# Kernel tuning notes

Measured on AMD Instinct MI355X. Metric: run time of the kernel, lower is better.

## Reference

```python
import jax, jax.numpy as jnp
import numpy as np
from jax import lax

B_, N_, DIM, HEADS, WS, HW = 16, 3136, 512, 8, 7, 56
SD = DIM // 2          # single_dim per branch (mul=[1,1])
S = SD // HEADS        # per-branch head dim


def setup_inputs() -> dict:
    key = jax.random.key(0)
    ks = jax.random.split(key, 12)
    r = lambda i, shape, sc=0.02: jax.random.normal(ks[i], shape, jnp.float32) * sc
    return dict(
        x=jax.random.normal(ks[0], (B_, N_, DIM), jnp.float32),
        H=HW, W=HW,
        q_w=r(1, (DIM, DIM)),
        kv_dw_w=r(2, (DIM, 1, 3, 3), 0.3), kv_dw_b=jnp.zeros((DIM,), jnp.float32),
        kv_pw_w=r(3, (DIM, DIM, 1, 1), 0.05), kv_pw_b=jnp.zeros((DIM,), jnp.float32),
        fc_w0=r(4, (S, S)), fc_w1=r(5, (S, S)),
        single_w0=r(6, (2 * S, S)), single_w1=r(7, (2 * S, S)),
        local_w0=r(8, (SD, 1, 3, 3), 0.3), local_b0=jnp.zeros((SD,), jnp.float32),
        local_w1=r(9, (SD, 1, 3, 3), 0.3), local_b1=jnp.zeros((SD,), jnp.float32),
        proj_w=r(10, (DIM, DIM)), proj_b=jnp.zeros((DIM,), jnp.float32),
    )


def _dwconv(x, w, b):
    # depthwise 3x3, padding 1 (NCHW / OIHW)
    y = lax.conv_general_dilated(x, w, (1, 1), [(1, 1), (1, 1)],
                                 feature_group_count=x.shape[1],
                                 dimension_numbers=('NCHW', 'OIHW', 'NCHW'))
    return y + b[None, :, None, None]


def _pwconv(x, w, b):
    y = lax.conv_general_dilated(x, w, (1, 1), [(0, 0), (0, 0)],
                                 dimension_numbers=('NCHW', 'OIHW', 'NCHW'))
    return y + b[None, :, None, None]


def _unfold(x, k, stride, dil):
    # nn.Unfold(kernel_size=k, stride=stride, padding=0, dilation=dil): [B,C,H,W] -> [B, C*k*k, L]
    B, C, H, W = x.shape
    L = (H - (dil * (k - 1) + 1)) // stride + 1  # H == W here
    idx = (jnp.arange(L) * stride)[:, None] + jnp.arange(k) * dil  # [L, k]
    t = x[:, :, idx, :]            # [B,C,Lh,kh,W]
    t = t[:, :, :, :, idx]         # [B,C,Lh,kh,Lw,kw]
    t = t.transpose(0, 1, 3, 5, 2, 4)  # [B,C,kh,kw,Lh,Lw] -> torch unfold channel order
    return t.reshape(B, C * k * k, L * L)


def reference(x, H, W, q_w, kv_dw_w, kv_dw_b, kv_pw_w, kv_pw_b,
              fc_w0, fc_w1, single_w0, single_w1,
              local_w0, local_b0, local_w1, local_b1, proj_w, proj_b):
    B, N, C = x.shape
    q = (x @ q_w.T).reshape(B, N, HEADS, C // HEADS).transpose(0, 2, 1, 3)  # [B,h,N,C/h]
    xim = x.reshape(B, H, W, C).transpose(0, 3, 1, 2)
    kv = _pwconv(_dwconv(xim, kv_dw_w, kv_dw_b), kv_pw_w, kv_pw_b)  # [B,C,H,W]
    branches = [(fc_w0, single_w0, local_w0, local_b0),
                (fc_w1, single_w1, local_w1, local_b1)]
    outs = []
    for i, (fc_w, single_w, lw, lb) in enumerate(branches):
        dil = 2 ** i
        stride = dil * (WS - 1) + 1
        q_ = q[:, :, :, i * S:(i + 1) * S]                      # [B,h,N,S]
        u = _unfold(kv[:, i * SD:(i + 1) * SD], WS, stride, dil)  # [B, SD*49, L]
        L = u.shape[-1]
        u = u.reshape(B, HEADS, S, WS * WS, L).transpose(0, 1, 3, 4, 2)  # [B,h,49,L,S]
        u = u.reshape(B, HEADS, WS * WS, L * S)
        # AdaptiveAvgPool2d((None, S)): mean over consecutive chunks of length L
        pooled = u.reshape(B, HEADS, WS * WS, S, L).mean(-1)     # [B,h,49,S]
        kvp = (pooled @ fc_w.T) @ single_w.T                     # [B,h,49,2S]
        k_, v_ = kvp[..., :S], kvp[..., S:]
        attn = jax.nn.softmax((q_ @ k_.transpose(0, 1, 3, 2)) * (S ** -0.5), axis=-1)  # [B,h,N,49]
        vimg = v_.transpose(0, 1, 3, 2).reshape(B, SD, WS, WS)
        v_ = v_ + _dwconv(vimg, lw, lb).reshape(B, HEADS, S, WS * WS).transpose(0, 1, 3, 2)
        outs.append((attn @ v_).transpose(0, 2, 1, 3).reshape(B, N, SD))
    return jnp.concatenate(outs, -1) @ proj_w.T + proj_b
```

## Files before the change

kernel.cpp:

```cpp
#include <hip/hip_runtime.h>


typedef _Float16 __attribute__((ext_vector_type(8))) f16x8;
typedef _Float16 __attribute__((ext_vector_type(4))) f16x4;
typedef float __attribute__((ext_vector_type(4))) f32x4;

#define NB    16
#define NTOK  3136
#define CDIM  512
#define HWDIM 56
#define SLICE 100352

__device__ __forceinline__ void gll16(const void* g, void* l) {
    __builtin_amdgcn_global_load_lds((const __attribute__((address_space(1))) void*)g,
                                     (__attribute__((address_space(3))) void*)l, 16, 0, 0);
}

__global__ __launch_bounds__(256) void cast_f2h(const float* __restrict__ in,
                                                _Float16* __restrict__ out, int n8) {
    int i = blockIdx.x * 256 + threadIdx.x;
    if (i >= n8) return;
    const float4* p = (const float4*)in + (size_t)i * 2;
    float4 a = p[0], b = p[1];
    f16x8 o;
    o[0] = (_Float16)a.x; o[1] = (_Float16)a.y; o[2] = (_Float16)a.z; o[3] = (_Float16)a.w;
    o[4] = (_Float16)b.x; o[5] = (_Float16)b.y; o[6] = (_Float16)b.z; o[7] = (_Float16)b.w;
    *(f16x8*)(out + (size_t)i * 8) = o;
}

__global__ __launch_bounds__(256) void prep(const float* __restrict__ q_w,
                                            const float* __restrict__ pw_w,
                                            const float* __restrict__ pj_w,
                                            const float* __restrict__ dw_w,
                                            _Float16* __restrict__ WQ,
                                            _Float16* __restrict__ WPW,
                                            _Float16* __restrict__ WPJ,
                                            float* __restrict__ WT) {
    int bid = blockIdx.x;
    if (bid < 384) {
        const float* src = bid < 128 ? q_w : (bid < 256 ? pw_w : pj_w);
        _Float16* dst = bid < 128 ? WQ : (bid < 256 ? WPW : WPJ);
        int i = (bid & 127) * 256 + threadIdx.x;
        const float4* p = (const float4*)src + (size_t)i * 2;
        float4 a = p[0], b = p[1];
        f16x8 o;
        o[0] = (_Float16)a.x; o[1] = (_Float16)a.y; o[2] = (_Float16)a.z; o[3] = (_Float16)a.w;
        o[4] = (_Float16)b.x; o[5] = (_Float16)b.y; o[6] = (_Float16)b.z; o[7] = (_Float16)b.w;
        *(f16x8*)(dst + (size_t)i * 8) = o;
    } else {
        int i = (bid - 384) * 256 + threadIdx.x;
        if (i < 512 * 9) {
            int c = i / 9, t = i - c * 9;
            WT[t * 512 + c] = dw_w[i];
        }
    }
}

__global__ __launch_bounds__(256) void dwconv3x3(const _Float16* __restrict__ xh,
                                                 const float* __restrict__ wt,
                                                 const float* __restrict__ bias,
                                                 _Float16* __restrict__ out) {
    const int pr = blockIdx.x * 4 + (threadIdx.x >> 6);
    const int c0 = (threadIdx.x & 63) * 8;
    const int b  = pr / (28 * HWDIM);
    const int rm = pr - b * (28 * HWDIM);
    const int hp = rm / HWDIM;
    const int w  = rm - hp * HWDIM;
    const int h0 = hp * 2;

    float wr[9][8];
#pragma unroll
    for (int t = 0; t < 9; ++t) {
        float4 a = *(const float4*)(wt + t * 512 + c0);
        float4 d = *(const float4*)(wt + t * 512 + c0 + 4);
        wr[t][0] = a.x; wr[t][1] = a.y; wr[t][2] = a.z; wr[t][3] = a.w;
        wr[t][4] = d.x; wr[t][5] = d.y; wr[t][6] = d.z; wr[t][7] = d.w;
    }
    float acc0[8], acc1[8];
    {
        float4 a = *(const float4*)(bias + c0);
        float4 d = *(const float4*)(bias + c0 + 4);
        acc0[0] = a.x; acc0[1] = a.y; acc0[2] = a.z; acc0[3] = a.w;
        acc0[4] = d.x; acc0[5] = d.y; acc0[6] = d.z; acc0[7] = d.w;
#pragma unroll
        for (int j = 0; j < 8; ++j) acc1[j] = acc0[j];
    }
#pragma unroll
    for (int rr = 0; rr < 4; ++rr) {
        const int row = h0 - 1 + rr;
        if ((unsigned)row >= HWDIM) continue;
#pragma unroll
        for (int kw = 0; kw < 3; ++kw) {
            const int ww = w + kw - 1;
            if ((unsigned)ww >= HWDIM) continue;
            f16x8 v = *(const f16x8*)(xh + ((size_t)(b * NTOK + row * HWDIM + ww) * CDIM + c0));
            if (rr < 3) {
                const int t = rr * 3 + kw;
#pragma unroll
                for (int j = 0; j < 8; ++j) acc0[j] += (float)v[j] * wr[t][j];
            }
            if (rr > 0) {
                const int t = (rr - 1) * 3 + kw;
#pragma unroll
                for (int j = 0; j < 8; ++j) acc1[j] += (float)v[j] * wr[t][j];
            }
        }
    }
    f16x8 o0, o1;
#pragma unroll
    for (int j = 0; j < 8; ++j) { o0[j] = (_Float16)acc0[j]; o1[j] = (_Float16)acc1[j]; }
    const size_t p0 = (size_t)(b * NTOK + h0 * HWDIM + w) * CDIM + c0;
    *(f16x8*)(out + p0) = o0;
    *(f16x8*)(out + p0 + (size_t)HWDIM * CDIM) = o1;
}

template <int MODE>
__global__ __launch_bounds__(256) void gemm_bt(const _Float16* __restrict__ A,
                                               const _Float16* __restrict__ B,
                                               const float* __restrict__ bias,
                                               _Float16* __restrict__ Ch,
                                               float* __restrict__ Cf,
                                               int M, int N, int K) {
    __shared__ _Float16 As[128 * 64];
    __shared__ _Float16 Bs[128 * 64];
    const int tid = threadIdx.x;
    const int lane = tid & 63;
    const int wave = tid >> 6;
    const size_t m0 = (size_t)blockIdx.x * 128;
    const int n0 = blockIdx.y * 128;
    const int wm = wave >> 1, wn = wave & 1;
    const int lr = lane & 15, lk = lane >> 4;
    const int srow = wave * 8 + (lane >> 3);
    const int scol = (lane & 7) * 8;

    unsigned bj[4], nj[4];
    const int shalf = scol >> 5;
    const int wcol = scol & 31;
    if constexpr (MODE == 2) {
#pragma unroll
        for (int j = 0; j < 4; ++j) {
            unsigned row = (unsigned)m0 + j * 32 + srow;
            bj[j] = row / 3136u;
            nj[j] = row - bj[j] * 3136u;
        }
    }

    f32x4 acc[4][4] = {};
    for (int kt = 0; kt < K; kt += 64) {
        if constexpr (MODE == 2) {
            const int s = (kt >> 5) + shalf;
            const size_t soff = (size_t)s * SLICE + wcol;
#pragma unroll
            for (int j = 0; j < 4; ++j) {
                gll16(A + (size_t)bj[j] * 16 * SLICE + soff + (size_t)nj[j] * 32,
                      &As[j * 2048 + wave * 512]);
                gll16(B + ((size_t)(n0 + j * 32 + srow) * K + kt + scol),
                      &Bs[j * 2048 + wave * 512]);
            }
        } else {
#pragma unroll
            for (int j = 0; j < 4; ++j) {
                gll16(A + ((m0 + j * 32 + srow) * K + kt + scol), &As[j * 2048 + wave * 512]);
                gll16(B + ((size_t)(n0 + j * 32 + srow) * K + kt + scol), &Bs[j * 2048 + wave * 512]);
            }
        }
        __syncthreads();
#pragma unroll
        for (int ks = 0; ks < 2; ++ks) {
            f16x8 af[4], bf[4];
#pragma unroll
            for (int mi = 0; mi < 4; ++mi)
                af[mi] = *(const f16x8*)&As[(wm * 64 + mi * 16 + lr) * 64 + ks * 32 + lk * 8];
#pragma unroll
            for (int ni = 0; ni < 4; ++ni)
                bf[ni] = *(const f16x8*)&Bs[(wn * 64 + ni * 16 + lr) * 64 + ks * 32 + lk * 8];
#pragma unroll
            for (int mi = 0; mi < 4; ++mi)
#pragma unroll
                for (int ni = 0; ni < 4; ++ni)
                    acc[mi][ni] = __builtin_amdgcn_mfma_f32_16x16x32_f16(af[mi], bf[ni], acc[mi][ni], 0, 0, 0);
        }
        __syncthreads();
    }

    if constexpr (MODE == 0) {
#pragma unroll
        for (int mi = 0; mi < 4; ++mi)
#pragma unroll
            for (int ni = 0; ni < 4; ++ni) {
                const int col = n0 + wn * 64 + ni * 16 + lr;
                const int sl = col >> 5, sc = col & 31;
#pragma unroll
                for (int j = 0; j < 4; ++j) {
                    unsigned row = (unsigned)m0 + wm * 64 + mi * 16 + lk * 4 + j;
                    unsigned bb = row / 3136u, nn = row - bb * 3136u;
                    Ch[((size_t)bb * 16 + sl) * SLICE + (size_t)nn * 32 + sc] =
                        (_Float16)acc[mi][ni][j];
                }
            }
    } else {
#pragma unroll
        for (int mi = 0; mi < 4; ++mi)
#pragma unroll
            for (int ni = 0; ni < 4; ++ni) {
                const int col = n0 + wn * 64 + ni * 16 + lr;
                const float bv = bias[col];
#pragma unroll
                for (int j = 0; j < 4; ++j) {
                    const size_t row = m0 + wm * 64 + mi * 16 + lk * 4 + j;
                    float v = acc[mi][ni][j] + bv;
                    if constexpr (MODE == 2) Cf[row * N + col] = v;
                    else Ch[row * N + col] = (_Float16)v;
                }
            }
    }
}

__global__ __launch_bounds__(256) void kv_small(const _Float16* __restrict__ kvh,
                                                const float* __restrict__ fc0, const float* __restrict__ fc1,
                                                const float* __restrict__ sg0, const float* __restrict__ sg1,
                                                const float* __restrict__ lw0, const float* __restrict__ lb0,
                                                const float* __restrict__ lw1, const float* __restrict__ lb1,
                                                _Float16* __restrict__ Kb, _Float16* __restrict__ Vb) {
    const int head = blockIdx.x;
    const int br = blockIdx.y;
    const int b = blockIdx.z;
    const float* fc = br ? fc1 : fc0;
    const float* sg = br ? sg1 : sg0;
    const float* lw = br ? lw1 : lw0;
    const float* lb = br ? lb1 : lb0;
    __shared__ float pooled[49 * 32];
    __shared__ float tmp[49 * 32];
    __shared__ float kvp[49 * 64];
    const int tid = threadIdx.x;
    if (br == 0) {
        for (int idx = tid; idx < 49 * 64; idx += 256) {
            int w = idx >> 6, l = idx & 63;
            int ly = l >> 3, lx = l & 7, pp = w / 7, qq = w % 7;
            int n = (ly * 7 + pp) * HWDIM + (lx * 7 + qq);
            const f16x8* src = (const f16x8*)(kvh + ((size_t)(b * NTOK + n) * CDIM + head * 32));
            float s = 0;
#pragma unroll
            for (int t = 0; t < 4; ++t) {
                f16x8 v = src[t];
#pragma unroll
                for (int j = 0; j < 8; ++j) s += (float)v[j];
            }
            kvp[idx] = s;
        }
        __syncthreads();
        for (int idx = tid; idx < 49 * 32; idx += 256) {
            int w = idx >> 5, sp = idx & 31;
            pooled[idx] = (kvp[(w << 6) + 2 * sp] + kvp[(w << 6) + 2 * sp + 1]) * (1.f / 64.f);
        }
    } else {
        for (int idx = tid; idx < 49 * 32; idx += 256) {
            int w = idx >> 5, t = idx & 31;
            int l = t >> 1, hf = t & 1;
            int ly = l >> 2, lx = l & 3, pp = w / 7, qq = w % 7;
            int n = (ly * 13 + pp * 2) * HWDIM + (lx * 13 + qq * 2);
            const f16x8* src = (const f16x8*)(kvh + ((size_t)(b * NTOK + n) * CDIM + 256 + head * 32 + hf * 16));
            float s = 0;
#pragma unroll
            for (int t2 = 0; t2 < 2; ++t2) {
                f16x8 v = src[t2];
#pragma unroll
                for (int j = 0; j < 8; ++j) s += (float)v[j];
            }
            pooled[idx] = s * (1.f / 16.f);
        }
    }
    __syncthreads();
    for (int idx = tid; idx < 49 * 32; idx += 256) {
        int w = idx >> 5, j = idx & 31;
        float s = 0;
#pragma unroll
        for (int k = 0; k < 32; ++k) s += pooled[(w << 5) + k] * fc[j * 32 + k];
        tmp[idx] = s;
    }
    __syncthreads();
    for (int idx = tid; idx < 49 * 64; idx += 256) {
        int w = idx >> 6, o = idx & 63;
        float s = 0;
#pragma unroll
        for (int k = 0; k < 32; ++k) s += tmp[(w << 5) + k] * sg[o * 32 + k];
        kvp[idx] = s;
    }
    __syncthreads();
    const size_t base = (((size_t)b * 2 + br) * 8 + head) * 1568;
    for (int idx = tid; idx < 49 * 32; idx += 256) {
        int w = idx >> 5, sp = idx & 31;
        Kb[base + idx] = (_Float16)kvp[(w << 6) + sp];
        int pp = w / 7, qq = w % 7;
        int c = head * 32 + sp;
        float a = kvp[(w << 6) + 32 + sp] + lb[c];
#pragma unroll
        for (int kh = 0; kh < 3; ++kh) {
            int p2 = pp + kh - 1;
            if ((unsigned)p2 >= 7) continue;
#pragma unroll
            for (int kw = 0; kw < 3; ++kw) {
                int q2 = qq + kw - 1;
                if ((unsigned)q2 >= 7) continue;
                a += kvp[((p2 * 7 + q2) << 6) + 32 + sp] * lw[c * 9 + kh * 3 + kw];
            }
        }
        Vb[base + idx] = (_Float16)a;
    }
}

__global__ __launch_bounds__(256) void attn_fused(const _Float16* __restrict__ Qp,
                                                  const _Float16* __restrict__ Kb,
                                                  const _Float16* __restrict__ Vb,
                                                  _Float16* __restrict__ AOp) {
    const int b = blockIdx.y;
    const int br = blockIdx.z >> 3;
    const int head = blockIdx.z & 7;
    __shared__ _Float16 Kp[64 * 40];
    __shared__ _Float16 Vt[32 * 72];
    __shared__ _Float16 Pw[4][32 * 72];
    const int tid = threadIdx.x;
    const int lane = tid & 63, wave = tid >> 6;
    const size_t kvbase = (((size_t)b * 2 + br) * 8 + head) * 1568;
    {
        int r = tid >> 2, ck = tid & 3;
        f16x8 v = {};
        if (r < 49) v = *(const f16x8*)(Kb + kvbase + r * 32 + ck * 8);
        *(f16x8*)&Kp[r * 40 + ck * 8] = v;
    }
    for (int idx = tid; idx < 64 * 32; idx += 256) {
        int w = idx >> 5, s = idx & 31;
        Vt[s * 72 + w] = (w < 49) ? Vb[kvbase + w * 32 + s] : (_Float16)0.f;
    }
    __syncthreads();
    const int mtile = blockIdx.x * 4 + wave;
    if (mtile >= 49) return;
    const int n0 = mtile * 64;
    const int lr = lane & 15, lk = lane >> 4;
    const size_t qsl = ((size_t)b * 16 + head * 2 + br) * SLICE + (size_t)n0 * 32;
    const size_t osl = ((size_t)b * 16 + br * 8 + head) * SLICE + (size_t)n0 * 32;

    f16x8 qf[4], kf[4];
#pragma unroll
    for (int mi = 0; mi < 4; ++mi)
        qf[mi] = *(const f16x8*)(Qp + qsl + (size_t)(mi * 16 + lr) * 32 + lk * 8);
#pragma unroll
    for (int ni = 0; ni < 4; ++ni)
        kf[ni] = *(const f16x8*)&Kp[(ni * 16 + lr) * 40 + lk * 8];
    f32x4 sacc[4][4] = {};
#pragma unroll
    for (int mi = 0; mi < 4; ++mi)
#pragma unroll
        for (int ni = 0; ni < 4; ++ni)
            sacc[mi][ni] = __builtin_amdgcn_mfma_f32_16x16x32_f16(qf[mi], kf[ni], sacc[mi][ni], 0, 0, 0);

    float den[4][4];
#pragma unroll
    for (int mi = 0; mi < 4; ++mi)
#pragma unroll
        for (int j = 0; j < 4; ++j) den[mi][j] = 0.f;
    const float SCALE = 0.17677669529663687f;
#pragma unroll
    for (int mi = 0; mi < 4; ++mi)
#pragma unroll
        for (int ni = 0; ni < 4; ++ni) {
            const bool valid = (ni * 16 + lr) < 49;
#pragma unroll
            for (int j = 0; j < 4; ++j) {
                float e = valid ? __expf(sacc[mi][ni][j] * SCALE) : 0.f;
                sacc[mi][ni][j] = e;
                den[mi][j] += e;
            }
        }
#pragma unroll
    for (int mi = 0; mi < 4; ++mi)
#pragma unroll
        for (int j = 0; j < 4; ++j) {
            float d = den[mi][j];
            d += __shfl_xor(d, 1);
            d += __shfl_xor(d, 2);
            d += __shfl_xor(d, 4);
            d += __shfl_xor(d, 8);
            den[mi][j] = 1.f / d;
        }
    f16x4 ph[4][4];
#pragma unroll
    for (int mi = 0; mi < 4; ++mi)
#pragma unroll
        for (int ni = 0; ni < 4; ++ni)
#pragma unroll
            for (int j = 0; j < 4; ++j)
                ph[mi][ni][j] = (_Float16)(sacc[mi][ni][j] * den[mi][j]);

    _Float16* P = Pw[wave];
#pragma unroll
    for (int h = 0; h < 2; ++h) {
#pragma unroll
        for (int mh = 0; mh < 2; ++mh) {
            const int mi = h * 2 + mh;
#pragma unroll
            for (int ni = 0; ni < 4; ++ni)
#pragma unroll
                for (int j = 0; j < 4; ++j)
                    P[(mh * 16 + lk * 4 + j) * 72 + ni * 16 + lr] = ph[mi][ni][j];
        }
        f32x4 oacc[2][2] = {};
#pragma unroll
        for (int k0 = 0; k0 < 2; ++k0) {
            f16x8 vf0 = *(const f16x8*)&Vt[lr * 72 + k0 * 32 + lk * 8];
            f16x8 vf1 = *(const f16x8*)&Vt[(16 + lr) * 72 + k0 * 32 + lk * 8];
#pragma unroll
            for (int mh = 0; mh < 2; ++mh) {
                f16x8 pf = *(const f16x8*)&P[(mh * 16 + lr) * 72 + k0 * 32 + lk * 8];
                oacc[mh][0] = __builtin_amdgcn_mfma_f32_16x16x32_f16(pf, vf0, oacc[mh][0], 0, 0, 0);
                oacc[mh][1] = __builtin_amdgcn_mfma_f32_16x16x32_f16(pf, vf1, oacc[mh][1], 0, 0, 0);
            }
        }
#pragma unroll
        for (int mh = 0; mh < 2; ++mh)
#pragma unroll
            for (int ci = 0; ci < 2; ++ci)
#pragma unroll
                for (int j = 0; j < 4; ++j)
                    P[(mh * 16 + lk * 4 + j) * 40 + ci * 16 + lr] = (_Float16)(oacc[mh][ci][j]);
#pragma unroll
        for (int t = 0; t < 2; ++t) {
            const int idx = t * 64 + lane;
            const int row = idx >> 2, ck = idx & 3;
            f16x8 ov = *(const f16x8*)&P[row * 40 + ck * 8];
            *(f16x8*)(AOp + osl + (size_t)(h * 32 + row) * 32 + ck * 8) = ov;
        }
    }
}

extern "C" void kernel_launch(void* const* d_in, const int* in_sizes, int n_in,
                              void* d_out, int out_size, void* d_ws, size_t ws_size,
                              hipStream_t stream) {
    const float* x       = (const float*)d_in[0];
    const float* q_w     = (const float*)d_in[3];
    const float* kv_dw_w = (const float*)d_in[4];
    const float* kv_dw_b = (const float*)d_in[5];
    const float* kv_pw_w = (const float*)d_in[6];
    const float* kv_pw_b = (const float*)d_in[7];
    const float* fc_w0   = (const float*)d_in[8];
    const float* fc_w1   = (const float*)d_in[9];
    const float* sg_w0   = (const float*)d_in[10];
    const float* sg_w1   = (const float*)d_in[11];
    const float* lw0     = (const float*)d_in[12];
    const float* lb0     = (const float*)d_in[13];
    const float* lw1     = (const float*)d_in[14];
    const float* lb1     = (const float*)d_in[15];
    const float* proj_w  = (const float*)d_in[16];
    const float* proj_b  = (const float*)d_in[17];

    char* ws = (char*)d_ws;
    const size_t SZ_BIG = (size_t)50176 * 512 * 2;
    _Float16* XH  = (_Float16*)(ws);
    _Float16* KVH = XH;
    _Float16* DW  = (_Float16*)(ws + SZ_BIG);
    _Float16* AO  = DW;
    _Float16* QH  = (_Float16*)(ws + 2 * SZ_BIG);
    _Float16* WQ  = (_Float16*)(ws + 3 * SZ_BIG);
    _Float16* WPW = WQ + 262144;
    _Float16* WPJ = WPW + 262144;
    _Float16* KB  = WPJ + 262144;
    _Float16* VB  = KB + (size_t)16 * 2 * 8 * 49 * 32;
    float*    WT  = (float*)(VB + (size_t)16 * 2 * 8 * 49 * 32);

    cast_f2h<<<dim3(12544), dim3(256), 0, stream>>>(x, XH, 25690112 / 8);
    prep<<<dim3(402), dim3(256), 0, stream>>>(q_w, kv_pw_w, proj_w, kv_dw_w, WQ, WPW, WPJ, WT);

    dwconv3x3<<<dim3(6272), dim3(256), 0, stream>>>(XH, WT, kv_dw_b, DW);

    gemm_bt<0><<<dim3(392, 4), dim3(256), 0, stream>>>(XH, WQ, nullptr, QH, nullptr, 50176, 512, 512);
    gemm_bt<1><<<dim3(392, 4), dim3(256), 0, stream>>>(DW, WPW, kv_pw_b, KVH, nullptr, 50176, 512, 512);

    kv_small<<<dim3(8, 2, 16), dim3(256), 0, stream>>>(KVH, fc_w0, fc_w1, sg_w0, sg_w1,
                                                       lw0, lb0, lw1, lb1, KB, VB);

    attn_fused<<<dim3(13, 16, 16), dim3(256), 0, stream>>>(QH, KB, VB, AO);

    gemm_bt<2><<<dim3(392, 4), dim3(256), 0, stream>>>(AO, WPJ, proj_b, nullptr, (float*)d_out,
                                                       50176, 512, 512);
}
```

Before: 486.1 us.

## Double-buffer GEMM LDS tiles with swizzle and N-fastest block order

Rewrites the shared gemm_bt main loop to use two 128x32 LDS buffers per operand. Global-to-LDS loads for step k+2 are issued while MFMAs run on step k, with explicit vmcnt waits and raw barriers instead of full syncthreads. It also XOR-swizzles the LDS column layout to reduce bank conflicts, raises wave priority around the MFMA block, and swaps the grid so the four N-tiles of one M row-block run adjacently for A-tile reuse in cache. The trade-off is a smaller K-step per barrier, which means more barriers per tile.

```diff
diff --git a/kernel.cpp b/kernel.cpp
--- a/kernel.cpp
+++ b/kernel.cpp
@@ -121,66 +121,72 @@
                                                _Float16* __restrict__ Ch,
                                                float* __restrict__ Cf,
                                                int M, int N, int K) {
-    __shared__ _Float16 As[128 * 64];
-    __shared__ _Float16 Bs[128 * 64];
-    const int tid = threadIdx.x;
+    __shared__ __align__(16) _Float16 As[2][128 * 32];
+    __shared__ __align__(16) _Float16 Bs[2][128 * 32];
+    const int tid  = threadIdx.x;
     const int lane = tid & 63;
     const int wave = tid >> 6;
-    const size_t m0 = (size_t)blockIdx.x * 128;
-    const int n0 = blockIdx.y * 128;
+    const size_t m0 = (size_t)blockIdx.y * 128;
+    const int    n0 = blockIdx.x * 128;
     const int wm = wave >> 1, wn = wave & 1;
     const int lr = lane & 15, lk = lane >> 4;
-    const int srow = wave * 8 + (lane >> 3);
-    const int scol = (lane & 7) * 8;
-
-    unsigned bj[4], nj[4];
-    const int shalf = scol >> 5;
-    const int wcol = scol & 31;
-    if constexpr (MODE == 2) {
-#pragma unroll
-        for (int j = 0; j < 4; ++j) {
-            unsigned row = (unsigned)m0 + j * 32 + srow;
-            bj[j] = row / 3136u;
-            nj[j] = row - bj[j] * 3136u;
-        }
-    }
+    const int srow0 = wave * 16 + (lane >> 2);
+    const int csw = ((lane & 3) ^ ((lane >> 3) & 3)) * 8;
+    const int kc  = (lk ^ ((lr >> 1) & 3)) * 8;
+    const int NK = K >> 5;
+    const int ldst = wave * 512;
+
+    size_t abase[2], bbase[2];
+#pragma unroll
+    for (int j = 0; j < 2; ++j) {
+        const int row = j * 64 + srow0;
+        if constexpr (MODE == 2) {
+            unsigned g = (unsigned)m0 + row;
+            unsigned bb = g / 3136u, nn = g - bb * 3136u;
+            abase[j] = ((size_t)bb * 16) * SLICE + (size_t)nn * 32 + csw;
+        } else {
+            abase[j] = (m0 + row) * (size_t)K + csw;
+        }
+        bbase[j] = (size_t)(n0 + row) * K + csw;
+    }
+
+    auto STAGE = [&](int t, int p) {
+#pragma unroll
+        for (int j = 0; j < 2; ++j) {
+            if constexpr (MODE == 2)
+                gll16(A + abase[j] + (size_t)t * SLICE, &As[p][j * 2048 + ldst]);
+            else
+                gll16(A + abase[j] + t * 32, &As[p][j * 2048 + ldst]);
+            gll16(B + bbase[j] + t * 32, &Bs[p][j * 2048 + ldst]);
+        }
+    };
 
     f32x4 acc[4][4] = {};
-    for (int kt = 0; kt < K; kt += 64) {
-        if constexpr (MODE == 2) {
-            const int s = (kt >> 5) + shalf;
-            const size_t soff = (size_t)s * SLICE + wcol;
-#pragma unroll
-            for (int j = 0; j < 4; ++j) {
-                gll16(A + (size_t)bj[j] * 16 * SLICE + soff + (size_t)nj[j] * 32,
-                      &As[j * 2048 + wave * 512]);
-                gll16(B + ((size_t)(n0 + j * 32 + srow) * K + kt + scol),
-                      &Bs[j * 2048 + wave * 512]);
-            }
-        } else {
-#pragma unroll
-            for (int j = 0; j < 4; ++j) {
-                gll16(A + ((m0 + j * 32 + srow) * K + kt + scol), &As[j * 2048 + wave * 512]);
-                gll16(B + ((size_t)(n0 + j * 32 + srow) * K + kt + scol), &Bs[j * 2048 + wave * 512]);
-            }
-        }
-        __syncthreads();
-#pragma unroll
-        for (int ks = 0; ks < 2; ++ks) {
-            f16x8 af[4], bf[4];
-#pragma unroll
-            for (int mi = 0; mi < 4; ++mi)
-                af[mi] = *(const f16x8*)&As[(wm * 64 + mi * 16 + lr) * 64 + ks * 32 + lk * 8];
+    STAGE(0, 0);
+    STAGE(1, 1);
+    for (int kt = 0; kt < NK; ++kt) {
+        const int p = kt & 1;
+        if (kt == NK - 1) asm volatile("s_waitcnt vmcnt(0)" ::: "memory");
+        else              asm volatile("s_waitcnt vmcnt(4)" ::: "memory");
+        __builtin_amdgcn_s_barrier();
+        __builtin_amdgcn_sched_barrier(0);
+        f16x8 af[4], bf[4];
+#pragma unroll
+        for (int mi = 0; mi < 4; ++mi)
+            af[mi] = *(const f16x8*)&As[p][(wm * 64 + mi * 16 + lr) * 32 + kc];
+#pragma unroll
+        for (int ni = 0; ni < 4; ++ni)
+            bf[ni] = *(const f16x8*)&Bs[p][(wn * 64 + ni * 16 + lr) * 32 + kc];
+        __builtin_amdgcn_s_setprio(1);
+#pragma unroll
+        for (int mi = 0; mi < 4; ++mi)
 #pragma unroll
             for (int ni = 0; ni < 4; ++ni)
-                bf[ni] = *(const f16x8*)&Bs[(wn * 64 + ni * 16 + lr) * 64 + ks * 32 + lk * 8];
-#pragma unroll
-            for (int mi = 0; mi < 4; ++mi)
-#pragma unroll
-                for (int ni = 0; ni < 4; ++ni)
-                    acc[mi][ni] = __builtin_amdgcn_mfma_f32_16x16x32_f16(af[mi], bf[ni], acc[mi][ni], 0, 0, 0);
-        }
-        __syncthreads();
+                acc[mi][ni] = __builtin_amdgcn_mfma_f32_16x16x32_f16(af[mi], bf[ni], acc[mi][ni], 0, 0, 0);
+        __builtin_amdgcn_s_setprio(0);
+        __builtin_amdgcn_sched_barrier(0);
+        __builtin_amdgcn_s_barrier();
+        if (kt < NK - 2) STAGE(kt + 2, p);
     }
 
     if constexpr (MODE == 0) {
@@ -472,14 +478,14 @@
 
     dwconv3x3<<<dim3(6272), dim3(256), 0, stream>>>(XH, WT, kv_dw_b, DW);
 
-    gemm_bt<0><<<dim3(392, 4), dim3(256), 0, stream>>>(XH, WQ, nullptr, QH, nullptr, 50176, 512, 512);
-    gemm_bt<1><<<dim3(392, 4), dim3(256), 0, stream>>>(DW, WPW, kv_pw_b, KVH, nullptr, 50176, 512, 512);
+    gemm_bt<0><<<dim3(4, 392), dim3(256), 0, stream>>>(XH, WQ, nullptr, QH, nullptr, 50176, 512, 512);
+    gemm_bt<1><<<dim3(4, 392), dim3(256), 0, stream>>>(DW, WPW, kv_pw_b, KVH, nullptr, 50176, 512, 512);
 
     kv_small<<<dim3(8, 2, 16), dim3(256), 0, stream>>>(KVH, fc_w0, fc_w1, sg_w0, sg_w1,
                                                        lw0, lb0, lw1, lb1, KB, VB);
 
     attn_fused<<<dim3(13, 16, 16), dim3(256), 0, stream>>>(QH, KB, VB, AO);
 
-    gemm_bt<2><<<dim3(392, 4), dim3(256), 0, stream>>>(AO, WPJ, proj_b, nullptr, (float*)d_out,
+    gemm_bt<2><<<dim3(4, 392), dim3(256), 0, stream>>>(AO, WPJ, proj_b, nullptr, (float*)d_out,
                                                        50176, 512, 512);
 }
```

Result: faster. 474.2 us (-2.5%).
